# Performance work log

Measured on AMD Instinct MI355X. Metric: run time of the kernel, lower is better.

## Reference

```python
import jax, jax.numpy as jnp
import numpy as np

B, Q, K, D, H = 16, 256, 256, 256, 256


def setup_inputs() -> dict:
    key = jax.random.key(0)
    ks = jax.random.split(key, 7)
    queries = jax.random.normal(ks[0], (B, Q, D), dtype=jnp.float32)
    keys = jax.random.normal(ks[1], (B, K, D), dtype=jnp.float32)
    values = jax.random.normal(ks[2], (B, K, D), dtype=jnp.float32)
    valid_lens = jax.random.randint(ks[3], (B,), 1, K + 1).astype(jnp.int64)
    # LazyLinear weights, no bias: W_q: D->H, W_k: D->H, w_v: H->1
    s = 1.0 / np.sqrt(D)
    Wq = jax.random.uniform(ks[4], (D, H), jnp.float32, -s, s)
    Wk = jax.random.uniform(ks[5], (D, H), jnp.float32, -s, s)
    sv = 1.0 / np.sqrt(H)
    wv = jax.random.uniform(ks[6], (H,), jnp.float32, -sv, sv)
    return {"queries": queries, "keys": keys, "values": values,
            "valid_lens": valid_lens, "Wq": Wq, "Wk": Wk, "wv": wv}


def reference(queries, keys, values, valid_lens, Wq, Wk, wv):
    q = queries @ Wq                      # [B,Q,H]
    k = keys @ Wk                         # [B,K,H]
    feats = jnp.tanh(q[:, :, None, :] + k[:, None, :, :])  # [B,Q,K,H]
    scores = jnp.einsum('bqkh,h->bqk', feats, wv)           # [B,Q,K]
    mask = jnp.arange(scores.shape[-1]) < valid_lens[:, None, None]  # [B,1,K]
    attn = jax.nn.softmax(jnp.where(mask, scores, -1e6), axis=-1)
    return jnp.einsum('bqk,bkv->bqv', attn, values)
```

## Files before the change

### kernel.cpp

```cpp
#include <hip/hip_runtime.h>

#define B_ 16
#define QN 256
#define KN 256
#define DN 256
#define HN 256

#define LOG2E 1.4426950408889634f
#define TWOLOG2E 2.8853900817779268f

__device__ inline float readlane_f(float v, int l) {
    return __uint_as_float(__builtin_amdgcn_readlane(__float_as_uint(v), l));
}

__global__ __launch_bounds__(256, 2) void proj_kernel(const float* __restrict__ Xq,
                                                      const float* __restrict__ Xk,
                                                      const float* __restrict__ Wq,
                                                      const float* __restrict__ Wk,
                                                      float* __restrict__ EQ,
                                                      float* __restrict__ EKT,
                                                      float scale) {
    const int nb = (int)gridDim.x >> 1;
    int blk = blockIdx.x;
    const bool is_q = blk < nb;
    const float* X;
    const float* W;
    if (is_q) { X = Xq; W = Wq; }
    else      { X = Xk; W = Wk; blk -= nb; }
    const int row0 = blk * 16;

    __shared__ float xl[16][260];
    __shared__ float trans[16][260];
    const int tid = threadIdx.x;

    {
        const float4* src = (const float4*)(X + (size_t)row0 * DN);
#pragma unroll
        for (int i = 0; i < 4; ++i) {
            int idx = tid + 256 * i;
            int r = idx >> 6, c = (idx & 63) << 2;
            *(float4*)&xl[r][c] = src[idx];
        }
    }
    __syncthreads();

    const int wvid = tid >> 6;
    const int rbase = (wvid >> 1) << 3;
    const int h2 = ((wvid & 1) << 7) | ((tid & 63) << 1);

    float2 acc[8];
#pragma unroll
    for (int r = 0; r < 8; ++r) acc[r] = make_float2(0.f, 0.f);

#define LOADW2(WS, D0)                                                         \
    do {                                                                       \
        _Pragma("unroll") for (int j = 0; j < 4; ++j)                          \
            WS[j] = *(const float2*)&W[(size_t)((D0) + j) * HN + h2];          \
    } while (0)

#define LOADX8(XS, D0)                                                         \
    do {                                                                       \
        _Pragma("unroll") for (int r = 0; r < 8; ++r)                          \
            XS[r] = *(const float4*)&xl[rbase + r][(D0)];                      \
    } while (0)

#define COMP2(WS, XS)                                                          \
    do {                                                                       \
        _Pragma("unroll") for (int r = 0; r < 8; ++r) {                        \
            acc[r].x = fmaf(XS[r].x, WS[0].x, acc[r].x);                       \
            acc[r].y = fmaf(XS[r].x, WS[0].y, acc[r].y);                       \
            acc[r].x = fmaf(XS[r].y, WS[1].x, acc[r].x);                       \
            acc[r].y = fmaf(XS[r].y, WS[1].y, acc[r].y);                       \
            acc[r].x = fmaf(XS[r].z, WS[2].x, acc[r].x);                       \
            acc[r].y = fmaf(XS[r].z, WS[2].y, acc[r].y);                       \
            acc[r].x = fmaf(XS[r].w, WS[3].x, acc[r].x);                       \
            acc[r].y = fmaf(XS[r].w, WS[3].y, acc[r].y);                       \
        }                                                                      \
    } while (0)

    {
        float2 w0[4], w1[4];
        float4 xA[8], xB[8];
        LOADX8(xA, 0);
        LOADX8(xB, 4);
        LOADW2(w0, 0);
        LOADW2(w1, 4);
        for (int d0 = 0; d0 < DN - 8; d0 += 8) {
            COMP2(w0, xA); LOADX8(xA, d0 + 8);  LOADW2(w0, d0 + 8);
            COMP2(w1, xB); LOADX8(xB, d0 + 12); LOADW2(w1, d0 + 12);
        }
        COMP2(w0, xA);
        COMP2(w1, xB);
    }

#pragma unroll
    for (int r = 0; r < 8; ++r) {
        acc[r].x = __builtin_amdgcn_exp2f(acc[r].x * scale);
        acc[r].y = __builtin_amdgcn_exp2f(acc[r].y * scale);
    }

    if (is_q) {
#pragma unroll
        for (int r = 0; r < 8; ++r)
            *(float2*)&EQ[(size_t)(row0 + rbase + r) * HN + h2] = acc[r];
    } else {
#pragma unroll
        for (int r = 0; r < 8; ++r)
            *(float2*)&trans[rbase + r][h2] = acc[r];
        __syncthreads();
        const int b = row0 >> 8, kloc0 = row0 & 255;
        float* dstb = EKT + (size_t)b * 32 * 256 * 8;
#pragma unroll
        for (int i = 0; i < 4; ++i) {
            int idx = i * 256 + tid;
            int u4 = (idx & 1) << 2;
            int kj = (idx >> 1) & 15;
            int h0 = idx >> 5;
            float4 val = *(const float4*)&trans[kj][h0 * 8 + u4];
            *(float4*)&dstb[((size_t)h0 * 256 + kloc0 + kj) * 8 + u4] = val;
        }
    }
}

__global__ __launch_bounds__(256, 8) void attn_kernel(const float* __restrict__ EQ,
                                                      const float* __restrict__ EKT,
                                                      const float* __restrict__ wv,
                                                      const int* __restrict__ lens,
                                                      const float* __restrict__ V,
                                                      float* __restrict__ OUT) {
    const int b = blockIdx.y;
    const int q0 = blockIdx.x * 2;
    const int len = lens[b];

    __shared__ float eq_lds[2][256];
    __shared__ float wv_lds[256];
    __shared__ float part[4][2][256];
    __shared__ float maxb[4][2];
    __shared__ float sumb[4][2];

    const int tid = threadIdx.x;
    const int w = tid >> 6, lane = tid & 63;

    {
        const float4* src = (const float4*)&EQ[((size_t)b * QN + q0) * HN];
        if (tid < 128) ((float4*)&eq_lds[0][0])[tid] = src[tid];
        if (tid >= 192) *(float4*)&wv_lds[(tid - 192) << 2] =
            ((const float4*)wv)[tid - 192];
    }
    __syncthreads();

    const bool act = (w * 64) < len;
    float acc[2] = {0.f, 0.f};

#define WINDOW(KA, KB, H8)                                                        \
    do {                                                                          \
        float4 wa = *(const float4*)&wv_lds[(H8)];                                \
        float4 wb = *(const float4*)&wv_lds[(H8) + 4];                            \
        _Pragma("unroll") for (int qq = 0; qq < 2; ++qq) {                        \
            float4 qa = *(const float4*)&eq_lds[qq][(H8)];                        \
            float4 qb = *(const float4*)&eq_lds[qq][(H8) + 4];                    \
            float t = acc[qq];                                                    \
            t = fmaf(wa.x, __builtin_amdgcn_rcpf(fmaf(qa.x, KA.x, 1.f)), t);      \
            t = fmaf(wa.y, __builtin_amdgcn_rcpf(fmaf(qa.y, KA.y, 1.f)), t);      \
            t = fmaf(wa.z, __builtin_amdgcn_rcpf(fmaf(qa.z, KA.z, 1.f)), t);      \
            t = fmaf(wa.w, __builtin_amdgcn_rcpf(fmaf(qa.w, KA.w, 1.f)), t);      \
            t = fmaf(wb.x, __builtin_amdgcn_rcpf(fmaf(qb.x, KB.x, 1.f)), t);      \
            t = fmaf(wb.y, __builtin_amdgcn_rcpf(fmaf(qb.y, KB.y, 1.f)), t);      \
            t = fmaf(wb.z, __builtin_amdgcn_rcpf(fmaf(qb.z, KB.z, 1.f)), t);      \
            t = fmaf(wb.w, __builtin_amdgcn_rcpf(fmaf(qb.w, KB.w, 1.f)), t);      \
            acc[qq] = t;                                                          \
        }                                                                         \
    } while (0)

    if (act) {
        const float* kp = EKT + (size_t)b * (32 * 256 * 8) + (size_t)(w * 64 + lane) * 8;
        float4 ka0 = *(const float4*)&kp[0];
        float4 kb0 = *(const float4*)&kp[4];
        float4 ka1, kb1;
        for (int hw = 0; hw < 32; hw += 2) {
            const float* kp1 = kp + (size_t)(hw + 1) * 2048;
            ka1 = *(const float4*)&kp1[0];
            kb1 = *(const float4*)&kp1[4];
            WINDOW(ka0, kb0, hw * 8);
            if (hw + 2 < 32) {
                const float* kp2 = kp + (size_t)(hw + 2) * 2048;
                ka0 = *(const float4*)&kp2[0];
                kb0 = *(const float4*)&kp2[4];
            }
            WINDOW(ka1, kb1, hw * 8 + 8);
        }
    }

    const bool kvalid = (w * 64 + lane) < len;
    float xs0 = kvalid ? (-2.f * acc[0]) : -1e6f;
    float xs1 = kvalid ? (-2.f * acc[1]) : -1e6f;

    float m0 = xs0, m1 = xs1;
#pragma unroll
    for (int off = 32; off; off >>= 1) {
        m0 = fmaxf(m0, __shfl_xor(m0, off, 64));
        m1 = fmaxf(m1, __shfl_xor(m1, off, 64));
    }
    if (lane == 0) { maxb[w][0] = m0; maxb[w][1] = m1; }
    __syncthreads();
    float g0 = fmaxf(fmaxf(maxb[0][0], maxb[1][0]), fmaxf(maxb[2][0], maxb[3][0]));
    float g1 = fmaxf(fmaxf(maxb[0][1], maxb[1][1]), fmaxf(maxb[2][1], maxb[3][1]));

    float p0 = __builtin_amdgcn_exp2f((xs0 - g0) * LOG2E);
    float p1 = __builtin_amdgcn_exp2f((xs1 - g1) * LOG2E);

    float s0 = p0, s1 = p1;
#pragma unroll
    for (int off = 32; off; off >>= 1) {
        s0 += __shfl_xor(s0, off, 64);
        s1 += __shfl_xor(s1, off, 64);
    }
    if (lane == 0) { sumb[w][0] = s0; sumb[w][1] = s1; }
    __syncthreads();
    float t0 = (sumb[0][0] + sumb[1][0]) + (sumb[2][0] + sumb[3][0]);
    float t1 = (sumb[0][1] + sumb[1][1]) + (sumb[2][1] + sumb[3][1]);
    p0 *= 1.f / t0;
    p1 *= 1.f / t1;

    float4 op0 = make_float4(0.f, 0.f, 0.f, 0.f);
    float4 op1 = op0;
    if (act) {
        int kmax = len - w * 64;
        if (kmax > 64) kmax = 64;
        const float* vb = V + ((size_t)b * KN + (size_t)w * 64) * DN + (lane << 2);

#define PV_STEP(KK, VV)                                                        \
    do {                                                                       \
        float b0 = readlane_f(p0, (KK));                                       \
        float b1 = readlane_f(p1, (KK));                                       \
        op0.x = fmaf(b0, VV.x, op0.x); op0.y = fmaf(b0, VV.y, op0.y);          \
        op0.z = fmaf(b0, VV.z, op0.z); op0.w = fmaf(b0, VV.w, op0.w);          \
        op1.x = fmaf(b1, VV.x, op1.x); op1.y = fmaf(b1, VV.y, op1.y);          \
        op1.z = fmaf(b1, VV.z, op1.z); op1.w = fmaf(b1, VV.w, op1.w);          \
    } while (0)

        int kk = 0;
        for (; kk + 4 <= kmax; kk += 4) {
            float4 v0 = *(const float4*)&vb[(size_t)(kk + 0) * DN];
            float4 v1 = *(const float4*)&vb[(size_t)(kk + 1) * DN];
            float4 v2 = *(const float4*)&vb[(size_t)(kk + 2) * DN];
            float4 v3 = *(const float4*)&vb[(size_t)(kk + 3) * DN];
            PV_STEP(kk + 0, v0);
            PV_STEP(kk + 1, v1);
            PV_STEP(kk + 2, v2);
            PV_STEP(kk + 3, v3);
        }
        for (; kk < kmax; ++kk) {
            float4 v0 = *(const float4*)&vb[(size_t)kk * DN];
            PV_STEP(kk, v0);
        }
    }
    {
        const int d4 = lane << 2;
        *(float4*)&part[w][0][d4] = op0;
        *(float4*)&part[w][1][d4] = op1;
    }
    __syncthreads();

    if (tid < 128) {
        const int q = tid >> 6, ln = tid & 63;
        const int d4 = ln << 2;
        float4 r0 = *(const float4*)&part[0][q][d4];
        float4 r1 = *(const float4*)&part[1][q][d4];
        float4 r2 = *(const float4*)&part[2][q][d4];
        float4 r3 = *(const float4*)&part[3][q][d4];
        float4 r = make_float4((r0.x + r1.x) + (r2.x + r3.x),
                               (r0.y + r1.y) + (r2.y + r3.y),
                               (r0.z + r1.z) + (r2.z + r3.z),
                               (r0.w + r1.w) + (r2.w + r3.w));
        *(float4*)&OUT[((size_t)b * QN + q0 + q) * DN + d4] = r;
    }
}

extern "C" void kernel_launch(void* const* d_in, const int* in_sizes, int n_in,
                              void* d_out, int out_size, void* d_ws, size_t ws_size,
                              hipStream_t stream) {
    const float* queries = (const float*)d_in[0];
    const float* keys    = (const float*)d_in[1];
    const float* values  = (const float*)d_in[2];
    const int*   lens    = (const int*)d_in[3];
    const float* Wq      = (const float*)d_in[4];
    const float* Wk      = (const float*)d_in[5];
    const float* wv      = (const float*)d_in[6];
    float* out = (float*)d_out;

    float* eq  = (float*)d_ws;
    float* ekT = eq + (size_t)B_ * QN * HN;

    proj_kernel<<<(B_ * QN + B_ * KN) / 16, 256, 0, stream>>>(
        queries, keys, Wq, Wk, eq, ekT, TWOLOG2E);

    dim3 gB(QN / 2, B_);
    attn_kernel<<<gB, 256, 0, stream>>>(eq, ekT, wv, lens, values, out);
}
```

Before: 56.28 us.

## Split score computation across waves by hidden dimension instead of key range

Each wave now handles a quarter of the hidden dimension for every active key chunk, rather than one 64-key chunk across all hidden dims. The aim is to keep all four waves busy when valid_len is short, where before waves covering masked keys sat idle. Per-wave partial scores are written to a shared buffer and summed after a barrier, and that buffer is reused for the output partials with an extra sync. This adds LDS traffic, an extra barrier and more live accumulators.

```diff
diff --git a/kernel.cpp b/kernel.cpp
--- a/kernel.cpp
+++ b/kernel.cpp
@@ -134,7 +134,7 @@
 
     __shared__ float eq_lds[2][256];
     __shared__ float wv_lds[256];
-    __shared__ float part[4][2][256];
+    __shared__ float shbuf[2048];
     __shared__ float maxb[4][2];
     __shared__ float sumb[4][2];
 
@@ -149,51 +149,87 @@
     }
     __syncthreads();
 
+    float a00 = 0.f, a01 = 0.f;
+    float a10 = 0.f, a11 = 0.f;
+    float a20 = 0.f, a21 = 0.f;
+    float a30 = 0.f, a31 = 0.f;
+
+    const float* ekb = EKT + (size_t)b * (32 * 256 * 8) + (size_t)(8 * w) * 2048;
+
+#define WINDOW(KA, KB, H8, A0, A1)                                               \
+    do {                                                                         \
+        float4 wa = *(const float4*)&wv_lds[(H8)];                               \
+        float4 wb = *(const float4*)&wv_lds[(H8) + 4];                           \
+        float4 qa0 = *(const float4*)&eq_lds[0][(H8)];                           \
+        float4 qb0 = *(const float4*)&eq_lds[0][(H8) + 4];                       \
+        float4 qa1 = *(const float4*)&eq_lds[1][(H8)];                           \
+        float4 qb1 = *(const float4*)&eq_lds[1][(H8) + 4];                       \
+        A0 = fmaf(wa.x, __builtin_amdgcn_rcpf(fmaf(qa0.x, KA.x, 1.f)), A0);      \
+        A0 = fmaf(wa.y, __builtin_amdgcn_rcpf(fmaf(qa0.y, KA.y, 1.f)), A0);      \
+        A0 = fmaf(wa.z, __builtin_amdgcn_rcpf(fmaf(qa0.z, KA.z, 1.f)), A0);      \
+        A0 = fmaf(wa.w, __builtin_amdgcn_rcpf(fmaf(qa0.w, KA.w, 1.f)), A0);      \
+        A0 = fmaf(wb.x, __builtin_amdgcn_rcpf(fmaf(qb0.x, KB.x, 1.f)), A0);      \
+        A0 = fmaf(wb.y, __builtin_amdgcn_rcpf(fmaf(qb0.y, KB.y, 1.f)), A0);      \
+        A0 = fmaf(wb.z, __builtin_amdgcn_rcpf(fmaf(qb0.z, KB.z, 1.f)), A0);      \
+        A0 = fmaf(wb.w, __builtin_amdgcn_rcpf(fmaf(qb0.w, KB.w, 1.f)), A0);      \
+        A1 = fmaf(wa.x, __builtin_amdgcn_rcpf(fmaf(qa1.x, KA.x, 1.f)), A1);      \
+        A1 = fmaf(wa.y, __builtin_amdgcn_rcpf(fmaf(qa1.y, KA.y, 1.f)), A1);      \
+        A1 = fmaf(wa.z, __builtin_amdgcn_rcpf(fmaf(qa1.z, KA.z, 1.f)), A1);      \
+        A1 = fmaf(wa.w, __builtin_amdgcn_rcpf(fmaf(qa1.w, KA.w, 1.f)), A1);      \
+        A1 = fmaf(wb.x, __builtin_amdgcn_rcpf(fmaf(qb1.x, KB.x, 1.f)), A1);      \
+        A1 = fmaf(wb.y, __builtin_amdgcn_rcpf(fmaf(qb1.y, KB.y, 1.f)), A1);      \
+        A1 = fmaf(wb.z, __builtin_amdgcn_rcpf(fmaf(qb1.z, KB.z, 1.f)), A1);      \
+        A1 = fmaf(wb.w, __builtin_amdgcn_rcpf(fmaf(qb1.w, KB.w, 1.f)), A1);      \
+    } while (0)
+
+#define PASS(J, A0, A1)                                                          \
+    do {                                                                         \
+        if ((J) * 64 < len) {                                                    \
+            const float* kp = ekb + (size_t)((J) * 64 + lane) * 8;               \
+            float4 ka0 = *(const float4*)&kp[0];                                 \
+            float4 kb0 = *(const float4*)&kp[4];                                 \
+            float4 ka1, kb1;                                                     \
+            _Pragma("unroll") for (int hw = 0; hw < 8; hw += 2) {                \
+                const float* kp1 = kp + (size_t)(hw + 1) * 2048;                 \
+                ka1 = *(const float4*)&kp1[0];                                   \
+                kb1 = *(const float4*)&kp1[4];                                   \
+                WINDOW(ka0, kb0, (w << 6) + hw * 8, A0, A1);                     \
+                if (hw + 2 < 8) {                                                \
+                    const float* kp2 = kp + (size_t)(hw + 2) * 2048;             \
+                    ka0 = *(const float4*)&kp2[0];                               \
+                    kb0 = *(const float4*)&kp2[4];                               \
+                }                                                                \
+                WINDOW(ka1, kb1, (w << 6) + hw * 8 + 8, A0, A1);                 \
+            }                                                                    \
+        }                                                                        \
+    } while (0)
+
+    PASS(0, a00, a01);
+    PASS(1, a10, a11);
+    PASS(2, a20, a21);
+    PASS(3, a30, a31);
+
+    {
+        float* sp = &shbuf[(size_t)(w << 3) * 64 + lane];
+        sp[0 * 64] = a00; sp[1 * 64] = a01;
+        sp[2 * 64] = a10; sp[3 * 64] = a11;
+        sp[4 * 64] = a20; sp[5 * 64] = a21;
+        sp[6 * 64] = a30; sp[7 * 64] = a31;
+    }
+    __syncthreads();
+
     const bool act = (w * 64) < len;
-    float acc[2] = {0.f, 0.f};
-
-#define WINDOW(KA, KB, H8)                                                        \
-    do {                                                                          \
-        float4 wa = *(const float4*)&wv_lds[(H8)];                                \
-        float4 wb = *(const float4*)&wv_lds[(H8) + 4];                            \
-        _Pragma("unroll") for (int qq = 0; qq < 2; ++qq) {                        \
-            float4 qa = *(const float4*)&eq_lds[qq][(H8)];                        \
-            float4 qb = *(const float4*)&eq_lds[qq][(H8) + 4];                    \
-            float t = acc[qq];                                                    \
-            t = fmaf(wa.x, __builtin_amdgcn_rcpf(fmaf(qa.x, KA.x, 1.f)), t);      \
-            t = fmaf(wa.y, __builtin_amdgcn_rcpf(fmaf(qa.y, KA.y, 1.f)), t);      \
-            t = fmaf(wa.z, __builtin_amdgcn_rcpf(fmaf(qa.z, KA.z, 1.f)), t);      \
-            t = fmaf(wa.w, __builtin_amdgcn_rcpf(fmaf(qa.w, KA.w, 1.f)), t);      \
-            t = fmaf(wb.x, __builtin_amdgcn_rcpf(fmaf(qb.x, KB.x, 1.f)), t);      \
-            t = fmaf(wb.y, __builtin_amdgcn_rcpf(fmaf(qb.y, KB.y, 1.f)), t);      \
-            t = fmaf(wb.z, __builtin_amdgcn_rcpf(fmaf(qb.z, KB.z, 1.f)), t);      \
-            t = fmaf(wb.w, __builtin_amdgcn_rcpf(fmaf(qb.w, KB.w, 1.f)), t);      \
-            acc[qq] = t;                                                          \
-        }                                                                         \
-    } while (0)
-
+    float sum0 = 0.f, sum1 = 0.f;
     if (act) {
-        const float* kp = EKT + (size_t)b * (32 * 256 * 8) + (size_t)(w * 64 + lane) * 8;
-        float4 ka0 = *(const float4*)&kp[0];
-        float4 kb0 = *(const float4*)&kp[4];
-        float4 ka1, kb1;
-        for (int hw = 0; hw < 32; hw += 2) {
-            const float* kp1 = kp + (size_t)(hw + 1) * 2048;
-            ka1 = *(const float4*)&kp1[0];
-            kb1 = *(const float4*)&kp1[4];
-            WINDOW(ka0, kb0, hw * 8);
-            if (hw + 2 < 32) {
-                const float* kp2 = kp + (size_t)(hw + 2) * 2048;
-                ka0 = *(const float4*)&kp2[0];
-                kb0 = *(const float4*)&kp2[4];
-            }
-            WINDOW(ka1, kb1, hw * 8 + 8);
-        }
-    }
-
+#pragma unroll
+        for (int hc = 0; hc < 4; ++hc) {
+            sum0 += shbuf[((hc * 4 + w) * 2 + 0) * 64 + lane];
+            sum1 += shbuf[((hc * 4 + w) * 2 + 1) * 64 + lane];
+        }
+    }
     const bool kvalid = (w * 64 + lane) < len;
-    float xs0 = kvalid ? (-2.f * acc[0]) : -1e6f;
-    float xs1 = kvalid ? (-2.f * acc[1]) : -1e6f;
+    float xs0 = kvalid ? (-2.f * sum0) : -1e6f;
+    float xs1 = kvalid ? (-2.f * sum1) : -1e6f;
 
     float m0 = xs0, m1 = xs1;
 #pragma unroll
@@ -255,20 +291,21 @@
             PV_STEP(kk, v0);
         }
     }
+    __syncthreads();
     {
         const int d4 = lane << 2;
-        *(float4*)&part[w][0][d4] = op0;
-        *(float4*)&part[w][1][d4] = op1;
+        *(float4*)&shbuf[((w << 1) + 0) * 256 + d4] = op0;
+        *(float4*)&shbuf[((w << 1) + 1) * 256 + d4] = op1;
     }
     __syncthreads();
 
     if (tid < 128) {
         const int q = tid >> 6, ln = tid & 63;
         const int d4 = ln << 2;
-        float4 r0 = *(const float4*)&part[0][q][d4];
-        float4 r1 = *(const float4*)&part[1][q][d4];
-        float4 r2 = *(const float4*)&part[2][q][d4];
-        float4 r3 = *(const float4*)&part[3][q][d4];
+        float4 r0 = *(const float4*)&shbuf[(0 * 2 + q) * 256 + d4];
+        float4 r1 = *(const float4*)&shbuf[(1 * 2 + q) * 256 + d4];
+        float4 r2 = *(const float4*)&shbuf[(2 * 2 + q) * 256 + d4];
+        float4 r3 = *(const float4*)&shbuf[(3 * 2 + q) * 256 + d4];
         float4 r = make_float4((r0.x + r1.x) + (r2.x + r3.x),
                                (r0.y + r1.y) + (r2.y + r3.y),
                                (r0.z + r1.z) + (r2.z + r3.z),
```

Result: faster. 54.83 us (-2.6%).
